# Optimization experiments

Hardware: AMD Instinct MI355X
Metric: run time of the kernel (lower is better)

## Reference

```python
import jax, jax.numpy as jnp
import numpy as np

ALPHA = 0.8  # STE clipping threshold (unused in fwd-only path)


def binary_sign(x):
    # torch: x.sign() with zeros mapped to +1 => where(x >= 0, 1, -1)
    return jnp.where(x >= 0, jnp.ones((), x.dtype), -jnp.ones((), x.dtype))


def setup_inputs() -> dict:
    key = jax.random.key(0)
    ks = jax.random.split(key, 5)
    B, D = 16384, 4096
    x = jax.random.normal(ks[0], (B, D), dtype=jnp.float32)
    w0 = jax.random.normal(ks[1], (D, D), dtype=jnp.float32) * 0.1
    w1 = jax.random.normal(ks[2], (D, D), dtype=jnp.float32) * 0.1
    w2 = jax.random.normal(ks[3], (D, D), dtype=jnp.float32) * 0.1
    w3 = jax.random.normal(ks[4], (1, D), dtype=jnp.float32) * 0.1
    b0 = jnp.zeros((D,), jnp.float32)
    b1 = jnp.zeros((D,), jnp.float32)
    b2 = jnp.zeros((D,), jnp.float32)
    b3 = jnp.zeros((1,), jnp.float32)
    return {"x": x, "w0": w0, "b0": b0, "w1": w1, "b1": b1,
            "w2": w2, "b2": b2, "w3": w3, "b3": b3}


def reference(x, w0, b0, w1, b1, w2, b2, w3, b3):
    h = x
    for w, b in ((w0, b0), (w1, b1), (w2, b2), (w3, b3)):
        # BinaryLinear: binarize weights, dense matmul, add bias
        z = jnp.einsum('bi,oi->bo', h, binary_sign(w)) + b
        # BinaryActivation: binarize pre-activation
        h = binary_sign(z)
    return h  # [B, 1]
```

## Files before the change

### kernel.cpp

```cpp
#include <hip/hip_runtime.h>

typedef int   v4i  __attribute__((ext_vector_type(4)));
typedef int   v16i __attribute__((ext_vector_type(16)));
typedef float f4   __attribute__((ext_vector_type(4)));

#define DD 4096
#define BATCH 16384

__device__ __forceinline__ void gload16(const void* g, void* l) {
  __builtin_amdgcn_global_load_lds((const __attribute__((address_space(1))) void*)g,
                                   (__attribute__((address_space(3))) void*)l, 16, 0, 0);
}
#define ASM_VMCNT(n) asm volatile("s_waitcnt vmcnt(" #n ")" ::: "memory")
#define ASM_LGKM0()  asm volatile("s_waitcnt lgkmcnt(0)" ::: "memory")
#define ASM_FENCE()  asm volatile("" ::: "memory")
#define BAR()        __builtin_amdgcn_s_barrier()


__global__ void binarize_swz_k(const float* __restrict__ w, unsigned char* __restrict__ o,
                               int swz_on) {
  int T = blockIdx.x * blockDim.x + threadIdx.x;
  int row = T >> 10, rem = T & 1023;
  int kblk = rem >> 4, seg = (rem >> 2) & 3, q = rem & 3;
  f4 v = *(const f4*)(w + (size_t)row * DD + kblk * 64 + seg * 16 + q * 4);
  unsigned int r = 0;
#pragma unroll
  for (int j = 0; j < 4; ++j) {
    unsigned int b = (v[j] >= 0.0f) ? 0x01u : 0xFFu;
    r |= b << (8 * j);
  }
  int slot = swz_on ? (seg ^ ((row >> 1) & 3)) : seg;
  *(unsigned int*)(o + (size_t)row * DD + kblk * 64 + slot * 16 + q * 4) = r;
}

__global__ void rowsum_k(const unsigned char* __restrict__ wb, int* __restrict__ R) {
  int lane = threadIdx.x & 63, wid = threadIdx.x >> 6;
  int row = blockIdx.x * 4 + wid;
  const unsigned char* p = wb + (size_t)row * DD;
  int s = 0;
#pragma unroll
  for (int j = 0; j < 4; ++j) {
    v4i a = *(const v4i*)(p + lane * 16 + j * 1024);
#pragma unroll
    for (int w = 0; w < 4; ++w) {
      unsigned int xa = (unsigned int)a[w];
#pragma unroll
      for (int by = 0; by < 4; ++by)
        s += (int)(signed char)((xa >> (8 * by)) & 255u);
    }
  }
#pragma unroll
  for (int off = 32; off > 0; off >>= 1) s += __shfl_down(s, off);
  if (lane == 0) R[row] = s;
}

__global__ void digitize_k(const float* __restrict__ x, unsigned char* __restrict__ Xd) {
  int T = blockIdx.x * blockDim.x + threadIdx.x;
  int row = T >> 10, rem = T & 1023;
  int kblk = rem >> 4, seg = (rem >> 2) & 3, q = rem & 3;
  f4 v = *(const f4*)(x + (size_t)row * DD + kblk * 64 + seg * 16 + q * 4);
  unsigned int Y[4];
#pragma unroll
  for (int j = 0; j < 4; ++j) {
    int X = (int)(v[j] * 134217728.0f);
    Y[j] = (unsigned int)(X + 1073741824);
  }
  size_t base = (size_t)row * 16384 + (size_t)kblk * 256;
  int r7 = row & 7;
#pragma unroll
  for (int d = 0; d < 4; ++d) {
    unsigned int wv = ((Y[0] >> (8 * d)) & 255u)
                    | (((Y[1] >> (8 * d)) & 255u) << 8)
                    | (((Y[2] >> (8 * d)) & 255u) << 16)
                    | (((Y[3] >> (8 * d)) & 255u) << 24);
    wv ^= 0x80808080u;
    int slot = ((d << 2) | seg) ^ r7;
    *(unsigned int*)(Xd + base + slot * 16 + q * 4) = wv;
  }
}

__global__ __launch_bounds__(256, 2) void gemm0p_k(
    const unsigned char* __restrict__ Xd, const unsigned char* __restrict__ wb,
    const int* __restrict__ R, const float* __restrict__ bias,
    signed char* __restrict__ h1) {
  __shared__ unsigned char As[2][64 * 256];
  __shared__ unsigned char Bs[2][128 * 64];
  const int tid = threadIdx.x, lane = tid & 63, wid = tid >> 6;
  const int wm = wid >> 1, wn = wid & 1;
  const int bid = blockIdx.x;
  const int xcd = bid & 7, sl = bid >> 3;
  const int m0 = ((xcd << 5) + (sl >> 5)) << 6;
  const int n0 = (sl & 31) << 7;

  v16i acc[4][2];
#pragma unroll
  for (int d = 0; d < 4; ++d)
#pragma unroll
    for (int f = 0; f < 2; ++f)
#pragma unroll
      for (int e = 0; e < 16; ++e) acc[d][f][e] = 0;

  auto stage = [&](int bf, int kb) {
#pragma unroll
    for (int i = 0; i < 4; ++i) {
      int c = wid * 4 + i;
      int lrow = c * 4 + (lane >> 4);
      const unsigned char* g = Xd + (size_t)(m0 + lrow) * 16384 + (size_t)kb * 256 + (lane & 15) * 16;
      gload16(g, &As[bf][c * 1024]);
    }
#pragma unroll
    for (int j = 0; j < 2; ++j) {
      int c = wid * 2 + j;
      int lrowB = c * 16 + (lane >> 2);
      const unsigned char* gB = wb + (size_t)(n0 + lrowB) * 4096 + kb * 64 + (lane & 3) * 16;
      gload16(gB, &Bs[bf][c * 1024]);
    }
  };

  auto compute = [&](int bf) {
    const int rl = lane & 31, hi = lane >> 5;
    const int arow = wm * 32 + rl;
    const int r7 = arow & 7;
#pragma unroll
    for (int kt = 0; kt < 2; ++kt) {
      int g = kt * 2 + hi;
      v4i a[4], b[2];
#pragma unroll
      for (int d = 0; d < 4; ++d) {
        int slot = ((d << 2) | g) ^ r7;
        a[d] = *(const v4i*)&As[bf][arow * 256 + slot * 16];
      }
#pragma unroll
      for (int f = 0; f < 2; ++f) {
        int brow = wn * 64 + f * 32 + rl;
        int slotb = g ^ ((brow >> 1) & 3);
        b[f] = *(const v4i*)&Bs[bf][brow * 64 + slotb * 16];
      }
#pragma unroll
      for (int d = 0; d < 4; ++d)
#pragma unroll
        for (int f = 0; f < 2; ++f)
          acc[d][f] = __builtin_amdgcn_mfma_i32_32x32x32_i8(a[d], b[f], acc[d][f], 0, 0, 0);
    }
  };

  stage(0, 0);
  stage(1, 1);
  ASM_VMCNT(6); BAR(); ASM_FENCE();
  int cur = 0;
  for (int t = 0; t < 64; ++t) {
    compute(cur);
    ASM_LGKM0(); BAR();
    if (t < 62) {
      stage(cur, t + 2);
      ASM_VMCNT(6); BAR(); ASM_FENCE();
    } else if (t == 62) {
      ASM_VMCNT(0); BAR(); ASM_FENCE();
    }
    cur ^= 1;
  }

#pragma unroll
  for (int f = 0; f < 2; ++f) {
    int col = n0 + wn * 64 + f * 32 + (lane & 31);
    long long rterm = 1082163328LL * (long long)R[col];
    double bb = (double)bias[col];
#pragma unroll
    for (int r = 0; r < 16; ++r) {
      long long Z = (long long)acc[0][f][r] + 256LL * (long long)acc[1][f][r]
                  + 65536LL * (long long)acc[2][f][r] + 16777216LL * (long long)acc[3][f][r]
                  + rterm;
      double z = (double)Z * 7.450580596923828125e-9 + bb;
      int row = m0 + wm * 32 + (r & 3) + 8 * (r >> 2) + 4 * (lane >> 5);
      int col2 = col ^ (((row >> 1) & 3) << 4);
      h1[(size_t)row * DD + col2] = (z >= 0.0) ? (signed char)1 : (signed char)(-1);
    }
  }
}

__global__ __launch_bounds__(512, 2) void gemm0f_k(
    const float* __restrict__ x, const unsigned char* __restrict__ wb,
    const int* __restrict__ R, const float* __restrict__ bias,
    signed char* __restrict__ h1) {
  __shared__ signed char As[2][4][128 * 80];
  __shared__ signed char Bs[2][128 * 80];
  const int tid = threadIdx.x;
  const int lane = tid & 63, wid = tid >> 6;
  const int wm = wid >> 1, wn = wid & 1;
  const int n0 = blockIdx.x * 128, m0 = blockIdx.y * 128;

  v16i acc[4][2];
#pragma unroll
  for (int d = 0; d < 4; ++d)
#pragma unroll
    for (int f = 0; f < 2; ++f)
#pragma unroll
      for (int e = 0; e < 16; ++e) acc[d][f][e] = 0;

  const int arow_l = tid >> 4, aseg = tid & 15;
  const int brow = tid >> 2,  bseg = (tid & 3) * 16;
  f4 va[4]; v4i vb;

  auto loadTile = [&](int kpos) {
#pragma unroll
    for (int p = 0; p < 4; ++p)
      va[p] = *(const f4*)(x + (size_t)(m0 + p * 32 + arow_l) * DD + kpos + aseg * 4);
    vb = *(const v4i*)(wb + (size_t)(n0 + brow) * DD + kpos + bseg);
  };
  auto writeTile = [&](int bf) {
#pragma unroll
    for (int p = 0; p < 4; ++p) {
      int row = p * 32 + arow_l;
      unsigned int Y[4];
#pragma unroll
      for (int j = 0; j < 4; ++j) {
        int X = (int)(va[p][j] * 134217728.0f);
        Y[j] = (unsigned int)(X + 1073741824);
      }
#pragma unroll
      for (int k = 0; k < 4; ++k) {
        unsigned int wv = ((Y[0] >> (8 * k)) & 255u) | (((Y[1] >> (8 * k)) & 255u) << 8)
                        | (((Y[2] >> (8 * k)) & 255u) << 16) | (((Y[3] >> (8 * k)) & 255u) << 24);
        wv ^= 0x80808080u;
        *(unsigned int*)&As[bf][k][row * 80 + aseg * 4] = wv;
      }
    }
    *(v4i*)&Bs[bf][brow * 80 + bseg] = vb;
  };

  loadTile(0); writeTile(0);
  __syncthreads();
  for (int t = 0; t < 64; ++t) {
    int cur = t & 1;
    if (t < 63) loadTile((t + 1) * 64);
#pragma unroll
    for (int kt = 0; kt < 2; ++kt) {
      int g = kt * 2 + (lane >> 5);
      int ar = (wm * 32 + (lane & 31)) * 80 + g * 16;
      v4i a[4], b[2];
#pragma unroll
      for (int d = 0; d < 4; ++d) a[d] = *(const v4i*)&As[cur][d][ar];
#pragma unroll
      for (int f = 0; f < 2; ++f) {
        int br = wn * 64 + f * 32 + (lane & 31);
        int slotb = g ^ ((br >> 1) & 3);
        b[f] = *(const v4i*)&Bs[cur][br * 80 + slotb * 16];
      }
#pragma unroll
      for (int d = 0; d < 4; ++d)
#pragma unroll
        for (int f = 0; f < 2; ++f)
          acc[d][f] = __builtin_amdgcn_mfma_i32_32x32x32_i8(a[d], b[f], acc[d][f], 0, 0, 0);
    }
    if (t < 63) writeTile(cur ^ 1);
    __syncthreads();
  }

#pragma unroll
  for (int f = 0; f < 2; ++f) {
    int col = n0 + wn * 64 + f * 32 + (lane & 31);
    long long rterm = 1082163328LL * (long long)R[col];
    double bb = (double)bias[col];
#pragma unroll
    for (int r = 0; r < 16; ++r) {
      long long Z = (long long)acc[0][f][r] + 256LL * (long long)acc[1][f][r]
                  + 65536LL * (long long)acc[2][f][r] + 16777216LL * (long long)acc[3][f][r]
                  + rterm;
      double z = (double)Z * 7.450580596923828125e-9 + bb;
      int row = m0 + wm * 32 + (r & 3) + 8 * (r >> 2) + 4 * (lane >> 5);
      int col2 = col ^ (((row >> 1) & 3) << 4);
      h1[(size_t)row * DD + col2] = (z >= 0.0) ? (signed char)1 : (signed char)(-1);
    }
  }
}

__global__ __launch_bounds__(256, 3) void gemm_bin_k(
    const unsigned char* __restrict__ A, const unsigned char* __restrict__ Bw,
    const float* __restrict__ bias, signed char* __restrict__ out) {
  __shared__ unsigned char As[2][128 * 64];
  __shared__ unsigned char Bs[2][128 * 64];
  const int tid = threadIdx.x, lane = tid & 63, wid = tid >> 6;
  const int wm = wid >> 1, wn = wid & 1;
  const int bid = blockIdx.x;
  const int xcd = bid & 7, sl = bid >> 3;
  const int m0 = ((xcd << 4) + (sl >> 5)) << 7;
  const int n0 = (sl & 31) << 7;

  v16i acc[2][2];
#pragma unroll
  for (int mi = 0; mi < 2; ++mi)
#pragma unroll
    for (int f = 0; f < 2; ++f)
#pragma unroll
      for (int e = 0; e < 16; ++e) acc[mi][f][e] = 0;

  auto stage = [&](int bf, int kb) {
#pragma unroll
    for (int j = 0; j < 2; ++j) {
      int c = wid * 2 + j;
      int lrow = c * 16 + (lane >> 2);
      const unsigned char* gA = A  + (size_t)(m0 + lrow) * 4096 + kb * 64 + (lane & 3) * 16;
      const unsigned char* gB = Bw + (size_t)(n0 + lrow) * 4096 + kb * 64 + (lane & 3) * 16;
      gload16(gA, &As[bf][c * 1024]);
      gload16(gB, &Bs[bf][c * 1024]);
    }
  };

  auto compute = [&](int bf) {
    const int rl = lane & 31, hi = lane >> 5;
#pragma unroll
    for (int kt = 0; kt < 2; ++kt) {
      int g = kt * 2 + hi;
      v4i a[2], b[2];
#pragma unroll
      for (int mi = 0; mi < 2; ++mi) {
        int arow = wm * 64 + mi * 32 + rl;
        int slot = g ^ ((arow >> 1) & 3);
        a[mi] = *(const v4i*)&As[bf][arow * 64 + slot * 16];
      }
#pragma unroll
      for (int f = 0; f < 2; ++f) {
        int brow = wn * 64 + f * 32 + rl;
        int slot = g ^ ((brow >> 1) & 3);
        b[f] = *(const v4i*)&Bs[bf][brow * 64 + slot * 16];
      }
#pragma unroll
      for (int mi = 0; mi < 2; ++mi)
#pragma unroll
        for (int f = 0; f < 2; ++f)
          acc[mi][f] = __builtin_amdgcn_mfma_i32_32x32x32_i8(a[mi], b[f], acc[mi][f], 0, 0, 0);
    }
  };

  stage(0, 0);
  stage(1, 1);
  ASM_VMCNT(4); BAR(); ASM_FENCE();
  int cur = 0;
  for (int t = 0; t < 64; ++t) {
    compute(cur);
    ASM_LGKM0(); BAR();
    if (t < 62) {
      stage(cur, t + 2);
      ASM_VMCNT(4); BAR(); ASM_FENCE();
    } else if (t == 62) {
      ASM_VMCNT(0); BAR(); ASM_FENCE();
    }
    cur ^= 1;
  }

#pragma unroll
  for (int mi = 0; mi < 2; ++mi)
#pragma unroll
    for (int f = 0; f < 2; ++f) {
      int col = n0 + wn * 64 + f * 32 + (lane & 31);
      float bb = bias[col];
#pragma unroll
      for (int r = 0; r < 16; ++r) {
        float z = (float)acc[mi][f][r] + bb;
        int row = m0 + wm * 64 + mi * 32 + (r & 3) + 8 * (r >> 2) + 4 * (lane >> 5);
        int col2 = col ^ (((row >> 1) & 3) << 4);
        out[(size_t)row * DD + col2] = (z >= 0.0f) ? (signed char)1 : (signed char)(-1);
      }
    }
}

__global__ void final_k(const unsigned char* __restrict__ h, const unsigned char* __restrict__ w3b,
                        const float* __restrict__ b3, float* __restrict__ out) {
  int lane = threadIdx.x & 63, wid = threadIdx.x >> 6;
  int row = blockIdx.x * 4 + wid;
  int swz = ((row >> 1) & 3) << 4;
  const unsigned char* p = h + (size_t)row * DD;
  int s = 0;
#pragma unroll
  for (int j = 0; j < 4; ++j) {
    int e = lane * 16 + j * 1024;
    v4i a = *(const v4i*)(p + (e ^ swz));
    v4i b = *(const v4i*)(w3b + e);
#pragma unroll
    for (int w = 0; w < 4; ++w) {
      unsigned int xa = (unsigned int)a[w], xb = (unsigned int)b[w];
#pragma unroll
      for (int by = 0; by < 4; ++by)
        s += (int)(signed char)((xa >> (8 * by)) & 255u)
           * (int)(signed char)((xb >> (8 * by)) & 255u);
    }
  }
#pragma unroll
  for (int off = 32; off > 0; off >>= 1) s += __shfl_down(s, off);
  if (lane == 0) {
    float z = (float)s + b3[0];
    out[row] = (z >= 0.0f) ? 1.0f : -1.0f;
  }
}

extern "C" void kernel_launch(void* const* d_in, const int* in_sizes, int n_in,
                              void* d_out, int out_size, void* d_ws, size_t ws_size,
                              hipStream_t stream) {
  (void)in_sizes; (void)n_in; (void)out_size;
  const float* x  = (const float*)d_in[0];
  const float* w0 = (const float*)d_in[1];
  const float* b0 = (const float*)d_in[2];
  const float* w1 = (const float*)d_in[3];
  const float* b1 = (const float*)d_in[4];
  const float* w2 = (const float*)d_in[5];
  const float* b2 = (const float*)d_in[6];
  const float* w3 = (const float*)d_in[7];
  const float* b3 = (const float*)d_in[8];

  char* ws = (char*)d_ws;
  unsigned char* w0b = (unsigned char*)(ws + 0);
  unsigned char* w1b = (unsigned char*)(ws + (16ull << 20));
  unsigned char* w2b = (unsigned char*)(ws + (32ull << 20));
  unsigned char* w3b = (unsigned char*)(ws + (48ull << 20));
  int*           R   = (int*)(ws + (48ull << 20) + 65536);
  unsigned char* h1  = (unsigned char*)(ws + (64ull << 20));
  unsigned char* h2  = (unsigned char*)(ws + (128ull << 20));
  unsigned char* Xd  = (unsigned char*)(ws + (128ull << 20));
  float* out = (float*)d_out;

  binarize_swz_k<<<16384, 256, 0, stream>>>(w0, w0b, 1);
  binarize_swz_k<<<16384, 256, 0, stream>>>(w1, w1b, 1);
  binarize_swz_k<<<16384, 256, 0, stream>>>(w2, w2b, 1);
  binarize_swz_k<<<4,     256, 0, stream>>>(w3, w3b, 0);
  rowsum_k<<<1024, 256, 0, stream>>>(w0b, R);

  if (ws_size >= (384ull << 20)) {
    digitize_k<<<65536, 256, 0, stream>>>(x, Xd);
    gemm0p_k<<<8192, 256, 0, stream>>>(Xd, w0b, R, b0, (signed char*)h1);
  } else {
    gemm0f_k<<<dim3(32, 128), 512, 0, stream>>>(x, w0b, R, b0, (signed char*)h1);
  }
  gemm_bin_k<<<4096, 256, 0, stream>>>(h1, w1b, b1, (signed char*)h2);
  gemm_bin_k<<<4096, 256, 0, stream>>>(h2, w2b, b2, (signed char*)h1);
  final_k<<<4096, 256, 0, stream>>>(h1, w3b, b3, out);
}
```

Baseline: 2.031 ms.

## Load full LDS tile into registers before issuing next stage, overlap loads with MFMA

In both int8 MFMA GEMM kernels, each k-step now reads all A/B fragments for the buffer into registers first. It then barriers and immediately issues the global-to-LDS prefetch into the freed buffer, so that prefetch overlaps the MFMA block. MFMAs are wrapped in s_setprio(1) to favour the compute wave, and the barrier uses an asm s_barrier with a memory clobber. This raises register pressure, since two k-slices of fragments are live at once, which could hurt occupancy.

```diff
diff --git a/kernel.cpp b/kernel.cpp
--- a/kernel.cpp
+++ b/kernel.cpp
@@ -13,8 +13,7 @@
 }
 #define ASM_VMCNT(n) asm volatile("s_waitcnt vmcnt(" #n ")" ::: "memory")
 #define ASM_LGKM0()  asm volatile("s_waitcnt lgkmcnt(0)" ::: "memory")
-#define ASM_FENCE()  asm volatile("" ::: "memory")
-#define BAR()        __builtin_amdgcn_s_barrier()
+#define BARF()       asm volatile("s_barrier" ::: "memory")
 
 
 __global__ void binarize_swz_k(const float* __restrict__ w, unsigned char* __restrict__ o,
@@ -117,46 +116,44 @@
     }
   };
 
-  auto compute = [&](int bf) {
-    const int rl = lane & 31, hi = lane >> 5;
-    const int arow = wm * 32 + rl;
-    const int r7 = arow & 7;
+  const int rl = lane & 31, hi = lane >> 5;
+  const int arow = wm * 32 + rl;
+  const int r7 = arow & 7;
+
+  stage(0, 0);
+  stage(1, 1);
+  ASM_VMCNT(6); BARF();
+  int cur = 0;
+  for (int t = 0; t < 64; ++t) {
+    v4i af[2][4], bg[2][2];
 #pragma unroll
     for (int kt = 0; kt < 2; ++kt) {
       int g = kt * 2 + hi;
-      v4i a[4], b[2];
 #pragma unroll
       for (int d = 0; d < 4; ++d) {
         int slot = ((d << 2) | g) ^ r7;
-        a[d] = *(const v4i*)&As[bf][arow * 256 + slot * 16];
+        af[kt][d] = *(const v4i*)&As[cur][arow * 256 + slot * 16];
       }
 #pragma unroll
       for (int f = 0; f < 2; ++f) {
         int brow = wn * 64 + f * 32 + rl;
         int slotb = g ^ ((brow >> 1) & 3);
-        b[f] = *(const v4i*)&Bs[bf][brow * 64 + slotb * 16];
-      }
+        bg[kt][f] = *(const v4i*)&Bs[cur][brow * 64 + slotb * 16];
+      }
+    }
+    ASM_LGKM0(); BARF();
+    if (t < 62) stage(cur, t + 2);
+    __builtin_amdgcn_s_setprio(1);
+#pragma unroll
+    for (int kt = 0; kt < 2; ++kt)
 #pragma unroll
       for (int d = 0; d < 4; ++d)
 #pragma unroll
         for (int f = 0; f < 2; ++f)
-          acc[d][f] = __builtin_amdgcn_mfma_i32_32x32x32_i8(a[d], b[f], acc[d][f], 0, 0, 0);
-    }
-  };
-
-  stage(0, 0);
-  stage(1, 1);
-  ASM_VMCNT(6); BAR(); ASM_FENCE();
-  int cur = 0;
-  for (int t = 0; t < 64; ++t) {
-    compute(cur);
-    ASM_LGKM0(); BAR();
-    if (t < 62) {
-      stage(cur, t + 2);
-      ASM_VMCNT(6); BAR(); ASM_FENCE();
-    } else if (t == 62) {
-      ASM_VMCNT(0); BAR(); ASM_FENCE();
-    }
+          acc[d][f] = __builtin_amdgcn_mfma_i32_32x32x32_i8(af[kt][d], bg[kt][f], acc[d][f], 0, 0, 0);
+    __builtin_amdgcn_s_setprio(0);
+    if (t < 62) { ASM_VMCNT(6); BARF(); }
+    else if (t == 62) { ASM_VMCNT(0); BARF(); }
     cur ^= 1;
   }
 
@@ -306,45 +303,43 @@
     }
   };
 
-  auto compute = [&](int bf) {
-    const int rl = lane & 31, hi = lane >> 5;
+  const int rl = lane & 31, hi = lane >> 5;
+
+  stage(0, 0);
+  stage(1, 1);
+  ASM_VMCNT(4); BARF();
+  int cur = 0;
+  for (int t = 0; t < 64; ++t) {
+    v4i af[2][2], bg[2][2];
 #pragma unroll
     for (int kt = 0; kt < 2; ++kt) {
       int g = kt * 2 + hi;
-      v4i a[2], b[2];
 #pragma unroll
       for (int mi = 0; mi < 2; ++mi) {
         int arow = wm * 64 + mi * 32 + rl;
         int slot = g ^ ((arow >> 1) & 3);
-        a[mi] = *(const v4i*)&As[bf][arow * 64 + slot * 16];
+        af[kt][mi] = *(const v4i*)&As[cur][arow * 64 + slot * 16];
       }
 #pragma unroll
       for (int f = 0; f < 2; ++f) {
         int brow = wn * 64 + f * 32 + rl;
         int slot = g ^ ((brow >> 1) & 3);
-        b[f] = *(const v4i*)&Bs[bf][brow * 64 + slot * 16];
-      }
+        bg[kt][f] = *(const v4i*)&Bs[cur][brow * 64 + slot * 16];
+      }
+    }
+    ASM_LGKM0(); BARF();
+    if (t < 62) stage(cur, t + 2);
+    __builtin_amdgcn_s_setprio(1);
+#pragma unroll
+    for (int kt = 0; kt < 2; ++kt)
 #pragma unroll
       for (int mi = 0; mi < 2; ++mi)
 #pragma unroll
         for (int f = 0; f < 2; ++f)
-          acc[mi][f] = __builtin_amdgcn_mfma_i32_32x32x32_i8(a[mi], b[f], acc[mi][f], 0, 0, 0);
-    }
-  };
-
-  stage(0, 0);
-  stage(1, 1);
-  ASM_VMCNT(4); BAR(); ASM_FENCE();
-  int cur = 0;
-  for (int t = 0; t < 64; ++t) {
-    compute(cur);
-    ASM_LGKM0(); BAR();
-    if (t < 62) {
-      stage(cur, t + 2);
-      ASM_VMCNT(4); BAR(); ASM_FENCE();
-    } else if (t == 62) {
-      ASM_VMCNT(0); BAR(); ASM_FENCE();
-    }
+          acc[mi][f] = __builtin_amdgcn_mfma_i32_32x32x32_i8(af[kt][mi], bg[kt][f], acc[mi][f], 0, 0, 0);
+    __builtin_amdgcn_s_setprio(0);
+    if (t < 62) { ASM_VMCNT(4); BARF(); }
+    else if (t == 62) { ASM_VMCNT(0); BARF(); }
     cur ^= 1;
   }
 
```

Result: faster. 1.927 ms (-5.1%).
